# Optimization experiments

Measured on AMD Instinct MI355X. Metric: run time of the kernel, lower is better.

Reference implementation:

```python
import jax, jax.numpy as jnp
import numpy as np

MAX_TIMESTEPS = 6
K_WTA = 1
THR_RATE = 0.05
OUT_CHANNELS = 128
TARGET_RATE = K_WTA / OUT_CHANNELS


def setup_inputs() -> dict:
    key = jax.random.key(0)
    kx, kw = jax.random.split(key)
    x = jax.random.normal(kx, (8, 128, 64, 64), dtype=jnp.float32)
    W = jax.random.normal(kw, (128, 256, 11, 11), dtype=jnp.float32)
    # per-output-filter L2 normalization as in __init__
    W = W / (1e-10 + jnp.sqrt(jnp.sum(W * W, axis=(1, 2, 3), keepdims=True)))
    return {"x": x, "W": W}


def _conv_same(x_in, W):
    return jax.lax.conv_general_dilated(
        x_in, W, window_strides=(1, 1), padding="SAME",
        dimension_numbers=("NCHW", "OIHW", "NCHW"))


def reference(x, W):
    B, C, H, Wd = x.shape
    Cout = W.shape[0]

    z0 = jnp.zeros((B, Cout, H, Wd), dtype=x.dtype)  # zeros_like(x), channels match
    b0 = jnp.zeros((1, Cout, 1, 1), dtype=x.dtype)

    def step(carry, t):
        z_prev, b = carry
        x_in = jnp.concatenate([x, z_prev], axis=1)          # [B, 2C, H, W]
        prelimy = _conv_same(x_in, W)                         # [B, Cout, H, W]
        realy = prelimy - b
        # EMA blend with previous (binarized) activation for t > 0
        realy = jnp.where(t > 0, 0.5 * realy + 0.5 * z_prev, realy)
        # k-WTA with k=1 over channel dim: keep only per-pixel channel max, binarize
        thr = jnp.max(realy, axis=1, keepdims=True)
        masked = jnp.where(realy < thr, 0.0, realy)
        z = (masked > 0).astype(x.dtype)
        # running sparsity-controlled bias update
        rate = jnp.mean(z, axis=(0, 2, 3)).reshape(1, -1, 1, 1)
        b = b + THR_RATE * (rate - TARGET_RATE)
        x_in_new = jnp.concatenate([x, z], axis=1)
        change = jnp.mean(jnp.abs(x_in - x_in_new))           # F.l1_loss
        return (z, b), (change, z)

    (_, _), (changes, zs) = jax.lax.scan(step, (z0, b0), jnp.arange(MAX_TIMESTEPS))
    features = jnp.transpose(zs, (1, 0, 2, 3, 4))             # [B, T, Cout, H, W]
    return changes, features
```

## Files before the change

kernel.cpp:

```cpp
#include <hip/hip_runtime.h>

typedef double d4 __attribute__((ext_vector_type(4)));

static constexpr int BN = 8;
static constexpr int CX = 128;
static constexpr int CO = 128;
static constexpr int HH = 64;
static constexpr int WW = 64;
static constexpr int KT = 121;
static constexpr int NPIX = HH * WW;
static constexpr int TOTPIX = BN * NPIX;

__global__ __launch_bounds__(128) void k_wt(const float* __restrict__ W,
                                            float* __restrict__ WxT,
                                            float* __restrict__ WzT) {
  int blk  = blockIdx.x;
  int part = blk >> 7;
  int ci   = blk & 127;
  int co   = threadIdx.x;
  const float* src = &W[((co * 256) + part * 128 + ci) * KT];
  float* dst = (part ? WzT : WxT) + ci * KT * 128 + co;
#pragma unroll 11
  for (int k = 0; k < KT; ++k) dst[k * 128] = src[k];
}

__global__ __launch_bounds__(256, 4) void k_conv(const float* __restrict__ x,
                                                 const float* __restrict__ WxT,
                                                 double* __restrict__ base) {
  int blk = blockIdx.x;
  int cog = blk & 7;
  int wt  = (blk >> 3) & 3;
  int ht  = (blk >> 5) & 3;
  int b   = blk >> 7;
  int H0 = ht * 16, W0 = wt * 16, CO0 = cog * 16;

  int tid  = threadIdx.x;
  int lane = tid & 63;
  int wv   = tid >> 6;
  int lg   = lane >> 4;
  int lc   = lane & 15;

  __shared__ double xs[2][42 * 28];
  __shared__ unsigned offtbl[124];

  if (tid < 124) {
    unsigned off;
    if (tid < 121) {
      int ki = tid / 11, kj = tid - ki * 11;
      off = (unsigned)(ki * 28 + kj);
    } else {
      off = (unsigned)(26 * 28);
    }
    offtbl[tid] = off;
  }
  for (int e = tid; e < 2 * 42 * 28; e += 256) (&xs[0][0])[e] = 0.0;

  d4 zz = {0., 0., 0., 0.};
  double amu  = (double)lc;
  double bsel = (lg == 0) ? 1.0 : 0.0;
  d4 pr = __builtin_amdgcn_mfma_f64_16x16x4f64(amu, bsel, zz, 0, 0, 0);
  d4 pc = __builtin_amdgcn_mfma_f64_16x16x4f64(bsel, amu, zz, 0, 0, 0);

  int e0 = tid, e1 = tid + 256, e2 = tid + 512;
  bool v0 = false, v1 = false, v2 = false;
  int g0 = 0, g1 = 0, g2 = 0;
  {
    int e = e0; int r = e / 28, cc = e - r * 28;
    int gh = H0 - 5 + r, gw = W0 - 5 + cc;
    v0 = (cc < 26) && ((unsigned)gh < 64u) && ((unsigned)gw < 64u);
    g0 = ((b * CX) * HH + gh) * WW + gw;
  }
  {
    int e = e1; int r = e / 28, cc = e - r * 28;
    int gh = H0 - 5 + r, gw = W0 - 5 + cc;
    v1 = (cc < 26) && ((unsigned)gh < 64u) && ((unsigned)gw < 64u);
    g1 = ((b * CX) * HH + gh) * WW + gw;
  }
  if (e2 < 728) {
    int e = e2; int r = e / 28, cc = e - r * 28;
    int gh = H0 - 5 + r, gw = W0 - 5 + cc;
    v2 = (cc < 26) && ((unsigned)gh < 64u) && ((unsigned)gw < 64u);
    g2 = ((b * CX) * HH + gh) * WW + gw;
  }

  float xv0 = 0.f, xv1 = 0.f, xv2 = 0.f;

  {
    if (v0) xv0 = x[g0];
    if (v1) xv1 = x[g1];
    if (v2) xv2 = x[g2];
    if (e0 < 728) xs[0][e0] = v0 ? (double)xv0 : 0.0;
    if (e1 < 728) xs[0][e1] = v1 ? (double)xv1 : 0.0;
    if (e2 < 728) xs[0][e2] = v2 ? (double)xv2 : 0.0;
  }
  __syncthreads();

  d4 acc0 = {0., 0., 0., 0.};
  d4 acc1 = {0., 0., 0., 0.};
  d4 acc2 = {0., 0., 0., 0.};
  d4 acc3 = {0., 0., 0., 0.};

  unsigned xbase = (unsigned)(wv * 112 + lc);
  double* xA = &xs[0][0];
  double* xB = &xs[1][0];

#define CONV_STEP(CI, XRD, XWR, LAST)                                        \
  {                                                                          \
    const float* wci = WxT + (CI) * (KT * 128) + CO0 + lc + lg * 128;        \
    const float* wcl = WxT + (CI) * (KT * 128) + 120 * 128 + CO0 + lc;       \
    float wf[31];                                                            \
    _Pragma("unroll")                                                        \
    for (int c = 0; c < 30; ++c) wf[c] = wci[c * 512];                       \
    {                                                                        \
      float vl = wcl[0];                                                     \
      wf[30] = (lg == 0) ? vl : 0.0f;        \
    }                                                                        \
    if (!(LAST)) {                                                           \
      int xo = ((CI) + 1) * (HH * WW);                                       \
      if (v0) xv0 = x[g0 + xo];                                              \
      if (v1) xv1 = x[g1 + xo];                                              \
      if (v2) xv2 = x[g2 + xo];                                              \
    }                                                                        \
    _Pragma("unroll")                                                        \
    for (int c = 0; c < 31; ++c) {                                           \
      double a = (double)wf[c];                                              \
      unsigned off = offtbl[c * 4 + lg];                                     \
      const double* bp = &(XRD)[xbase + off];                                \
      double b0 = bp[0];                                                     \
      double b1 = bp[28];                                                    \
      double b2 = bp[56];                                                    \
      double b3 = bp[84];                                                    \
      acc0 = __builtin_amdgcn_mfma_f64_16x16x4f64(a, b0, acc0, 0, 0, 0);     \
      acc1 = __builtin_amdgcn_mfma_f64_16x16x4f64(a, b1, acc1, 0, 0, 0);     \
      acc2 = __builtin_amdgcn_mfma_f64_16x16x4f64(a, b2, acc2, 0, 0, 0);     \
      acc3 = __builtin_amdgcn_mfma_f64_16x16x4f64(a, b3, acc3, 0, 0, 0);     \
    }                                                                        \
    if (!(LAST)) {                                                           \
      if (e0 < 728) (XWR)[e0] = v0 ? (double)xv0 : 0.0;                      \
      if (e1 < 728) (XWR)[e1] = v1 ? (double)xv1 : 0.0;                      \
      if (e2 < 728) (XWR)[e2] = v2 ? (double)xv2 : 0.0;                      \
    }                                                                        \
    __syncthreads();                                                         \
  }

  for (int ci = 0; ci < 126; ci += 2) {
    CONV_STEP(ci, xA, xB, false)
    CONV_STEP(ci + 1, xB, xA, false)
  }
  CONV_STEP(126, xA, xB, false)
  CONV_STEP(127, xB, xA, true)
#undef CONV_STEP

  int hbase = H0 + wv * 4;
#pragma unroll
  for (int i = 0; i < 4; ++i) {
    int co = CO0 + (int)pr[i];
    int wc = W0 + (int)pc[i];
    double* dst = &base[((size_t)b * NPIX + hbase * 64 + wc) * 128 + co];
    dst[0 * 8192] = acc0[i];
    dst[1 * 8192] = acc1[i];
    dst[2 * 8192] = acc2[i];
    dst[3 * 8192] = acc3[i];
  }
}

__global__ __launch_bounds__(256) void k_step(
    const double* __restrict__ base, const float* __restrict__ WzT,
    const unsigned int* __restrict__ counts,
    unsigned int* __restrict__ countsT,
    unsigned int* __restrict__ chgT,
    const unsigned char* __restrict__ widxPrev,
    unsigned char* __restrict__ widxCur,
    const float* __restrict__ zf, int t) {
  int wv   = threadIdx.x >> 6;
  int lane = threadIdx.x & 63;
  int hp   = lane >> 5;
  int l32  = lane & 31;
  int slot = (wv << 1) + hp;
  int pix  = (blockIdx.x << 3) + slot;
  int b  = pix >> 12;
  int hw = pix & 4095;
  int h = hw >> 6, w = hw & 63;
  int co0 = l32 << 2;

  __shared__ int nbrS[8][121];

  double bias0 = 0.0, bias1 = 0.0, bias2 = 0.0, bias3 = 0.0;
  for (int s = 0; s < t; ++s) {
    uint4 cv = *reinterpret_cast<const uint4*>(&counts[s * 128 + co0]);
    bias0 += 0.05 * ((double)cv.x * (1.0 / 32768.0) - 1.0 / 128.0);
    bias1 += 0.05 * ((double)cv.y * (1.0 / 32768.0) - 1.0 / 128.0);
    bias2 += 0.05 * ((double)cv.z * (1.0 / 32768.0) - 1.0 / 128.0);
    bias3 += 0.05 * ((double)cv.w * (1.0 / 32768.0) - 1.0 / 128.0);
  }

  if (t > 0) {
#pragma unroll
    for (int q = 0; q < 4; ++q) {
      int k = l32 + q * 32;
      if (k < 121) {
        int ki = k / 11, kj = k - ki * 11;
        int nh = h + ki - 5, nw = w + kj - 5;
        int c = 255;
        if ((unsigned)nh < 64u && (unsigned)nw < 64u)
          c = (int)widxPrev[(b << 12) + (nh << 6) + nw];
        nbrS[slot][k] = c;
      }
    }
  }
  __syncthreads();

  double r0, r1, r2, r3;
  {
    const double* bp_ = &base[(size_t)pix * 128 + co0];
    double2 bb0 = *reinterpret_cast<const double2*>(bp_);
    double2 bb1 = *reinterpret_cast<const double2*>(bp_ + 2);
    r0 = bb0.x; r1 = bb0.y; r2 = bb1.x; r3 = bb1.y;
  }

  const float4* zf4 = reinterpret_cast<const float4*>(zf);
  int wpc = 255;
  if (t > 0) {
    const int* nb = nbrS[slot];
    wpc = nb[60];
    double ap[4][4] = {};
#pragma unroll 6
    for (int k = 0; k < 120; k += 4) {
      int c0 = nb[k], c1 = nb[k + 1], c2 = nb[k + 2], c3 = nb[k + 3];
      const float4* q0 = (c0 < 128)
          ? reinterpret_cast<const float4*>(&WzT[((c0 * KT + k) << 7) + co0])
          : zf4;
      const float4* q1 = (c1 < 128)
          ? reinterpret_cast<const float4*>(&WzT[((c1 * KT + k + 1) << 7) + co0])
          : zf4;
      const float4* q2 = (c2 < 128)
          ? reinterpret_cast<const float4*>(&WzT[((c2 * KT + k + 2) << 7) + co0])
          : zf4;
      const float4* q3 = (c3 < 128)
          ? reinterpret_cast<const float4*>(&WzT[((c3 * KT + k + 3) << 7) + co0])
          : zf4;
      float4 f0 = *q0, f1 = *q1, f2 = *q2, f3 = *q3;
      ap[0][0] += (double)f0.x; ap[0][1] += (double)f0.y;
      ap[0][2] += (double)f0.z; ap[0][3] += (double)f0.w;
      ap[1][0] += (double)f1.x; ap[1][1] += (double)f1.y;
      ap[1][2] += (double)f1.z; ap[1][3] += (double)f1.w;
      ap[2][0] += (double)f2.x; ap[2][1] += (double)f2.y;
      ap[2][2] += (double)f2.z; ap[2][3] += (double)f2.w;
      ap[3][0] += (double)f3.x; ap[3][1] += (double)f3.y;
      ap[3][2] += (double)f3.z; ap[3][3] += (double)f3.w;
    }
    int cl = nb[120];
    const float4* ql = (cl < 128)
        ? reinterpret_cast<const float4*>(&WzT[((cl * KT + 120) << 7) + co0])
        : zf4;
    float4 fl = *ql;
    ap[0][0] += (double)fl.x; ap[0][1] += (double)fl.y;
    ap[0][2] += (double)fl.z; ap[0][3] += (double)fl.w;
    r0 += (ap[0][0] + ap[1][0]) + (ap[2][0] + ap[3][0]);
    r1 += (ap[0][1] + ap[1][1]) + (ap[2][1] + ap[3][1]);
    r2 += (ap[0][2] + ap[1][2]) + (ap[2][2] + ap[3][2]);
    r3 += (ap[0][3] + ap[1][3]) + (ap[2][3] + ap[3][3]);
  }

  r0 -= bias0; r1 -= bias1; r2 -= bias2; r3 -= bias3;
  if (t > 0) {
    r0 = 0.5 * r0 + ((wpc == co0)     ? 0.5 : 0.0);
    r1 = 0.5 * r1 + ((wpc == co0 + 1) ? 0.5 : 0.0);
    r2 = 0.5 * r2 + ((wpc == co0 + 2) ? 0.5 : 0.0);
    r3 = 0.5 * r3 + ((wpc == co0 + 3) ? 0.5 : 0.0);
  }

  double m = fmax(fmax(r0, r1), fmax(r2, r3));
#pragma unroll
  for (int s = 1; s < 32; s <<= 1) m = fmax(m, __shfl_xor(m, s, 32));

  int cand = 255;
  if ((r3 == m) && (r3 > 0.0)) cand = co0 + 3;
  if ((r2 == m) && (r2 > 0.0)) cand = co0 + 2;
  if ((r1 == m) && (r1 > 0.0)) cand = co0 + 1;
  if ((r0 == m) && (r0 > 0.0)) cand = co0;
#pragma unroll
  for (int s = 1; s < 32; s <<= 1) {
    int o = __shfl_xor(cand, s, 32);
    cand = (o < cand) ? o : cand;
  }

  if (l32 == 0) {
    int wi = cand;
    widxCur[pix] = (unsigned char)wi;
    if (wi < 128) atomicAdd(&countsT[wi], 1u);
    if (wpc != wi)
      atomicAdd(chgT, (unsigned)((wpc != 255) + (wi != 255)));
  }
}

__global__ __launch_bounds__(64) void k_ch(const unsigned int* __restrict__ chg,
                                           float* __restrict__ outCh) {
  int t = threadIdx.x;
  if (t < 6) outCh[t] = (float)((double)chg[t] * (1.0 / 8388608.0));
}

__global__ __launch_bounds__(256) void k_feat(const unsigned char* __restrict__ widxA,
                                              float* __restrict__ featBase) {
  int idx = blockIdx.x * 256 + threadIdx.x;
  int hw4 = idx & 1023;
  int co  = (idx >> 10) & 127;
  int bt  = idx >> 17;
  int t = bt % 6, b = bt / 6;
  const unsigned char* wp = &widxA[(size_t)(t * BN + b) * 4096 + hw4 * 4];
  float4 o;
  o.x = (wp[0] == co) ? 1.f : 0.f;
  o.y = (wp[1] == co) ? 1.f : 0.f;
  o.z = (wp[2] == co) ? 1.f : 0.f;
  o.w = (wp[3] == co) ? 1.f : 0.f;
  *reinterpret_cast<float4*>(&featBase[(size_t)idx * 4]) = o;
}

extern "C" void kernel_launch(void* const* d_in, const int* in_sizes, int n_in,
                              void* d_out, int out_size, void* d_ws, size_t ws_size,
                              hipStream_t stream) {
  const float* x = (const float*)d_in[0];
  const float* W = (const float*)d_in[1];
  float* out = (float*)d_out;

  char* ws = (char*)d_ws;
  float* WxT = (float*)ws;
  float* WzT = (float*)(ws + 7929856);
  double* base = (double*)(ws + 2 * 7929856);
  char* p = ws + 2 * 7929856 + 33554432;
  unsigned int* counts = (unsigned int*)p; p += 6 * 128 * 4;
  unsigned int* chg = (unsigned int*)p;    p += 128;
  float* zf = (float*)p;                   p += 64;
  unsigned char* widxA = (unsigned char*)p;

  hipMemsetAsync(counts, 0, 3264, stream);

  k_wt<<<256, 128, 0, stream>>>(W, WxT, WzT);
  k_conv<<<1024, 256, 0, stream>>>(x, WxT, base);

  for (int t = 0; t < 6; ++t) {
    unsigned char* wc = widxA + (size_t)t * TOTPIX;
    const unsigned char* wp = (t > 0) ? (widxA + (size_t)(t - 1) * TOTPIX)
                                      : widxA;
    k_step<<<4096, 256, 0, stream>>>(base, WzT, counts, counts + t * 128,
                                     chg + t, wp, wc, zf, t);
  }
  k_ch<<<1, 64, 0, stream>>>(chg, out);
  k_feat<<<24576, 256, 0, stream>>>(widxA, out + 6);
}
```

Baseline: 2.786 ms.

## Give each wavefront a private input halo tile to drop block barriers

```diff
diff --git a/kernel.cpp b/kernel.cpp
--- a/kernel.cpp
+++ b/kernel.cpp
@@ -40,7 +40,7 @@
   int lg   = lane >> 4;
   int lc   = lane & 15;
 
-  __shared__ double xs[2][42 * 28];
+  __shared__ double xs[4][2][504];
   __shared__ unsigned offtbl[124];
 
   if (tid < 124) {
@@ -49,11 +49,11 @@
       int ki = tid / 11, kj = tid - ki * 11;
       off = (unsigned)(ki * 28 + kj);
     } else {
-      off = (unsigned)(26 * 28);
+      off = (unsigned)(14 * 28);
     }
     offtbl[tid] = off;
   }
-  for (int e = tid; e < 2 * 42 * 28; e += 256) (&xs[0][0])[e] = 0.0;
+  for (int e = tid; e < 4 * 2 * 504; e += 256) (&xs[0][0][0])[e] = 0.0;
 
   d4 zz = {0., 0., 0., 0.};
   double amu  = (double)lc;
@@ -61,48 +61,38 @@
   d4 pr = __builtin_amdgcn_mfma_f64_16x16x4f64(amu, bsel, zz, 0, 0, 0);
   d4 pc = __builtin_amdgcn_mfma_f64_16x16x4f64(bsel, amu, zz, 0, 0, 0);
 
-  int e0 = tid, e1 = tid + 256, e2 = tid + 512;
-  bool v0 = false, v1 = false, v2 = false;
-  int g0 = 0, g1 = 0, g2 = 0;
+  unsigned vm = 0;
+  int gs[7];
+#pragma unroll
+  for (int s = 0; s < 7; ++s) {
+    int e = lane + 64 * s;
+    int r = e / 28, cc = e - r * 28;
+    int gh = H0 + wv * 4 - 5 + r;
+    int gw = W0 - 5 + cc;
+    bool v = (e < 392) && (cc < 26) && ((unsigned)gh < 64u) &&
+             ((unsigned)gw < 64u);
+    vm |= (v ? 1u : 0u) << s;
+    gs[s] = ((b * CX) * HH + gh) * WW + gw;
+  }
+
+  __syncthreads();
+
+  double* xA = &xs[wv][0][0];
+  double* xB = &xs[wv][1][0];
+
   {
-    int e = e0; int r = e / 28, cc = e - r * 28;
-    int gh = H0 - 5 + r, gw = W0 - 5 + cc;
-    v0 = (cc < 26) && ((unsigned)gh < 64u) && ((unsigned)gw < 64u);
-    g0 = ((b * CX) * HH + gh) * WW + gw;
-  }
-  {
-    int e = e1; int r = e / 28, cc = e - r * 28;
-    int gh = H0 - 5 + r, gw = W0 - 5 + cc;
-    v1 = (cc < 26) && ((unsigned)gh < 64u) && ((unsigned)gw < 64u);
-    g1 = ((b * CX) * HH + gh) * WW + gw;
-  }
-  if (e2 < 728) {
-    int e = e2; int r = e / 28, cc = e - r * 28;
-    int gh = H0 - 5 + r, gw = W0 - 5 + cc;
-    v2 = (cc < 26) && ((unsigned)gh < 64u) && ((unsigned)gw < 64u);
-    g2 = ((b * CX) * HH + gh) * WW + gw;
-  }
-
-  float xv0 = 0.f, xv1 = 0.f, xv2 = 0.f;
-
-  {
-    if (v0) xv0 = x[g0];
-    if (v1) xv1 = x[g1];
-    if (v2) xv2 = x[g2];
-    if (e0 < 728) xs[0][e0] = v0 ? (double)xv0 : 0.0;
-    if (e1 < 728) xs[0][e1] = v1 ? (double)xv1 : 0.0;
-    if (e2 < 728) xs[0][e2] = v2 ? (double)xv2 : 0.0;
-  }
-  __syncthreads();
+#pragma unroll
+    for (int s = 0; s < 7; ++s) {
+      float xv = 0.f;
+      if ((vm >> s) & 1) xv = x[gs[s]];
+      xA[lane + 64 * s] = ((vm >> s) & 1) ? (double)xv : 0.0;
+    }
+  }
 
   d4 acc0 = {0., 0., 0., 0.};
   d4 acc1 = {0., 0., 0., 0.};
   d4 acc2 = {0., 0., 0., 0.};
   d4 acc3 = {0., 0., 0., 0.};
-
-  unsigned xbase = (unsigned)(wv * 112 + lc);
-  double* xA = &xs[0][0];
-  double* xB = &xs[1][0];
 
 #define CONV_STEP(CI, XRD, XWR, LAST)                                        \
   {                                                                          \
@@ -115,17 +105,20 @@
       float vl = wcl[0];                                                     \
       wf[30] = (lg == 0) ? vl : 0.0f;        \
     }                                                                        \
+    float xv[7];                                                             \
     if (!(LAST)) {                                                           \
       int xo = ((CI) + 1) * (HH * WW);                                       \
-      if (v0) xv0 = x[g0 + xo];                                              \
-      if (v1) xv1 = x[g1 + xo];                                              \
-      if (v2) xv2 = x[g2 + xo];                                              \
+      _Pragma("unroll")                                                      \
+      for (int s = 0; s < 7; ++s) {                                          \
+        xv[s] = 0.f;                                                         \
+        if ((vm >> s) & 1) xv[s] = x[gs[s] + xo];                            \
+      }                                                                      \
     }                                                                        \
     _Pragma("unroll")                                                        \
     for (int c = 0; c < 31; ++c) {                                           \
       double a = (double)wf[c];                                              \
       unsigned off = offtbl[c * 4 + lg];                                     \
-      const double* bp = &(XRD)[xbase + off];                                \
+      const double* bp = &(XRD)[lc + off];                                   \
       double b0 = bp[0];                                                     \
       double b1 = bp[28];                                                    \
       double b2 = bp[56];                                                    \
@@ -136,11 +129,10 @@
       acc3 = __builtin_amdgcn_mfma_f64_16x16x4f64(a, b3, acc3, 0, 0, 0);     \
     }                                                                        \
     if (!(LAST)) {                                                           \
-      if (e0 < 728) (XWR)[e0] = v0 ? (double)xv0 : 0.0;                      \
-      if (e1 < 728) (XWR)[e1] = v1 ? (double)xv1 : 0.0;                      \
-      if (e2 < 728) (XWR)[e2] = v2 ? (double)xv2 : 0.0;                      \
+      _Pragma("unroll")                                                      \
+      for (int s = 0; s < 7; ++s)                                            \
+        (XWR)[lane + 64 * s] = ((vm >> s) & 1) ? (double)xv[s] : 0.0;        \
     }                                                                        \
-    __syncthreads();                                                         \
   }
 
   for (int ci = 0; ci < 126; ci += 2) {
```

Result: slower. 2.844 ms (+2.1%).

## Stage conv weights in shared memory and drop double-buffered input tile

Applied to the files above, without the earlier changes.

```diff
diff --git a/kernel.cpp b/kernel.cpp
--- a/kernel.cpp
+++ b/kernel.cpp
@@ -40,7 +40,8 @@
   int lg   = lane >> 4;
   int lc   = lane & 15;
 
-  __shared__ double xs[2][42 * 28];
+  __shared__ double xs[42 * 28];
+  __shared__ double wsl[124 * 16];
   __shared__ unsigned offtbl[124];
 
   if (tid < 124) {
@@ -53,7 +54,8 @@
     }
     offtbl[tid] = off;
   }
-  for (int e = tid; e < 2 * 42 * 28; e += 256) (&xs[0][0])[e] = 0.0;
+  for (int e = tid; e < 42 * 28; e += 256) xs[e] = 0.0;
+  if (tid < 48) wsl[121 * 16 + tid] = 0.0;
 
   d4 zz = {0., 0., 0., 0.};
   double amu  = (double)lc;
@@ -82,16 +84,31 @@
     v2 = (cc < 26) && ((unsigned)gh < 64u) && ((unsigned)gw < 64u);
     g2 = ((b * CX) * HH + gh) * WW + gw;
   }
+  bool wact = (tid < 242);
+  int wk = tid >> 1;
+  int wgoff = wk * 128 + CO0 + (tid & 1) * 8;
 
   float xv0 = 0.f, xv1 = 0.f, xv2 = 0.f;
+  float4 wva = {0, 0, 0, 0}, wvb = {0, 0, 0, 0};
 
   {
     if (v0) xv0 = x[g0];
     if (v1) xv1 = x[g1];
     if (v2) xv2 = x[g2];
-    if (e0 < 728) xs[0][e0] = v0 ? (double)xv0 : 0.0;
-    if (e1 < 728) xs[0][e1] = v1 ? (double)xv1 : 0.0;
-    if (e2 < 728) xs[0][e2] = v2 ? (double)xv2 : 0.0;
+    if (wact) {
+      wva = *reinterpret_cast<const float4*>(&WxT[wgoff]);
+      wvb = *reinterpret_cast<const float4*>(&WxT[wgoff + 4]);
+    }
+    if (e0 < 728) xs[e0] = v0 ? (double)xv0 : 0.0;
+    if (e1 < 728) xs[e1] = v1 ? (double)xv1 : 0.0;
+    if (e2 < 728) xs[e2] = v2 ? (double)xv2 : 0.0;
+    if (wact) {
+      double* dst = &wsl[wk * 16 + (tid & 1) * 8];
+      dst[0] = (double)wva.x; dst[1] = (double)wva.y;
+      dst[2] = (double)wva.z; dst[3] = (double)wva.w;
+      dst[4] = (double)wvb.x; dst[5] = (double)wvb.y;
+      dst[6] = (double)wvb.z; dst[7] = (double)wvb.w;
+    }
   }
   __syncthreads();
 
@@ -101,55 +118,50 @@
   d4 acc3 = {0., 0., 0., 0.};
 
   unsigned xbase = (unsigned)(wv * 112 + lc);
-  double* xA = &xs[0][0];
-  double* xB = &xs[1][0];
-
-#define CONV_STEP(CI, XRD, XWR, LAST)                                        \
-  {                                                                          \
-    const float* wci = WxT + (CI) * (KT * 128) + CO0 + lc + lg * 128;        \
-    const float* wcl = WxT + (CI) * (KT * 128) + 120 * 128 + CO0 + lc;       \
-    float wf[31];                                                            \
-    _Pragma("unroll")                                                        \
-    for (int c = 0; c < 30; ++c) wf[c] = wci[c * 512];                       \
-    {                                                                        \
-      float vl = wcl[0];                                                     \
-      wf[30] = (lg == 0) ? vl : 0.0f;        \
-    }                                                                        \
-    if (!(LAST)) {                                                           \
-      int xo = ((CI) + 1) * (HH * WW);                                       \
-      if (v0) xv0 = x[g0 + xo];                                              \
-      if (v1) xv1 = x[g1 + xo];                                              \
-      if (v2) xv2 = x[g2 + xo];                                              \
-    }                                                                        \
-    _Pragma("unroll")                                                        \
-    for (int c = 0; c < 31; ++c) {                                           \
-      double a = (double)wf[c];                                              \
-      unsigned off = offtbl[c * 4 + lg];                                     \
-      const double* bp = &(XRD)[xbase + off];                                \
-      double b0 = bp[0];                                                     \
-      double b1 = bp[28];                                                    \
-      double b2 = bp[56];                                                    \
-      double b3 = bp[84];                                                    \
-      acc0 = __builtin_amdgcn_mfma_f64_16x16x4f64(a, b0, acc0, 0, 0, 0);     \
-      acc1 = __builtin_amdgcn_mfma_f64_16x16x4f64(a, b1, acc1, 0, 0, 0);     \
-      acc2 = __builtin_amdgcn_mfma_f64_16x16x4f64(a, b2, acc2, 0, 0, 0);     \
-      acc3 = __builtin_amdgcn_mfma_f64_16x16x4f64(a, b3, acc3, 0, 0, 0);     \
-    }                                                                        \
-    if (!(LAST)) {                                                           \
-      if (e0 < 728) (XWR)[e0] = v0 ? (double)xv0 : 0.0;                      \
-      if (e1 < 728) (XWR)[e1] = v1 ? (double)xv1 : 0.0;                      \
-      if (e2 < 728) (XWR)[e2] = v2 ? (double)xv2 : 0.0;                      \
-    }                                                                        \
-    __syncthreads();                                                         \
-  }
-
-  for (int ci = 0; ci < 126; ci += 2) {
-    CONV_STEP(ci, xA, xB, false)
-    CONV_STEP(ci + 1, xB, xA, false)
-  }
-  CONV_STEP(126, xA, xB, false)
-  CONV_STEP(127, xB, xA, true)
-#undef CONV_STEP
+
+  for (int ci = 0; ci < CX; ++ci) {
+    if (ci < CX - 1) {
+      int xo = (ci + 1) * (HH * WW);
+      int wo = (ci + 1) * (KT * 128);
+      if (v0) xv0 = x[g0 + xo];
+      if (v1) xv1 = x[g1 + xo];
+      if (v2) xv2 = x[g2 + xo];
+      if (wact) {
+        wva = *reinterpret_cast<const float4*>(&WxT[wo + wgoff]);
+        wvb = *reinterpret_cast<const float4*>(&WxT[wo + wgoff + 4]);
+      }
+    }
+
+#pragma unroll 31
+    for (int c = 0; c < 31; ++c) {
+      double a = wsl[(unsigned)(c * 64 + lg * 16 + lc)];
+      unsigned off = offtbl[(unsigned)(c * 4 + lg)];
+      const double* bp = &xs[xbase + off];
+      double b0 = bp[0];
+      double b1 = bp[28];
+      double b2 = bp[56];
+      double b3 = bp[84];
+      acc0 = __builtin_amdgcn_mfma_f64_16x16x4f64(a, b0, acc0, 0, 0, 0);
+      acc1 = __builtin_amdgcn_mfma_f64_16x16x4f64(a, b1, acc1, 0, 0, 0);
+      acc2 = __builtin_amdgcn_mfma_f64_16x16x4f64(a, b2, acc2, 0, 0, 0);
+      acc3 = __builtin_amdgcn_mfma_f64_16x16x4f64(a, b3, acc3, 0, 0, 0);
+    }
+    __syncthreads();
+
+    if (ci < CX - 1) {
+      if (e0 < 728) xs[e0] = v0 ? (double)xv0 : 0.0;
+      if (e1 < 728) xs[e1] = v1 ? (double)xv1 : 0.0;
+      if (e2 < 728) xs[e2] = v2 ? (double)xv2 : 0.0;
+      if (wact) {
+        double* dst = &wsl[wk * 16 + (tid & 1) * 8];
+        dst[0] = (double)wva.x; dst[1] = (double)wva.y;
+        dst[2] = (double)wva.z; dst[3] = (double)wva.w;
+        dst[4] = (double)wvb.x; dst[5] = (double)wvb.y;
+        dst[6] = (double)wvb.z; dst[7] = (double)wvb.w;
+      }
+      __syncthreads();
+    }
+  }
 
   int hbase = H0 + wv * 4;
 #pragma unroll
```

Measured after the change: 2.747 ms. Within noise of the previous version (-1.4%).
